# Kernel optimization log

Measured on AMD Instinct MI355X. Metric: run time of the kernel, lower is better.

Reference implementation:

```python
import jax, jax.numpy as jnp
import numpy as np

HIDDEN_STATE_CLAMP = 4.0
MAX_REVIEW_LENGTH = 200
B, T, D_IN, D_H, D_OUT = 1024, 200, 300, 256, 2


def setup_inputs() -> dict:
    key = jax.random.key(0)
    k_x, k_wh, k_bh, k_wo, k_bo = jax.random.split(key, 5)
    fan_h = D_IN + D_H
    inputs = jax.random.normal(k_x, (B, T, D_IN), dtype=jnp.float32)
    # torch nn.Linear init: U(-1/sqrt(fan_in), 1/sqrt(fan_in)); stored as [in, out] here
    Wh = jax.random.uniform(k_wh, (fan_h, D_H), jnp.float32, -1.0, 1.0) / np.sqrt(fan_h)
    bh = jax.random.uniform(k_bh, (D_H,), jnp.float32, -1.0, 1.0) / np.sqrt(fan_h)
    Wo = jax.random.uniform(k_wo, (D_H, D_OUT), jnp.float32, -1.0, 1.0) / np.sqrt(D_H)
    bo = jax.random.uniform(k_bo, (D_OUT,), jnp.float32, -1.0, 1.0) / np.sqrt(D_H)
    return {"inputs": inputs, "Wh": Wh, "bh": bh, "Wo": Wo, "bo": bo}


def reference(inputs, Wh, bh, Wo, bo):
    # inputs: [B, T, D_in]; process at most MAX_REVIEW_LENGTH timesteps
    x_t = jnp.swapaxes(inputs[:, :MAX_REVIEW_LENGTH], 0, 1)  # [T, B, D_in]
    h0 = jnp.zeros((inputs.shape[0], Wh.shape[1]), dtype=inputs.dtype)

    def step(h, xt):
        combined = jnp.concatenate([xt, h], axis=-1)          # [B, D_in+D_h]
        pre = combined @ Wh + bh
        h = jnp.tanh(jnp.clip(pre, -HIDDEN_STATE_CLAMP, HIDDEN_STATE_CLAMP))
        return h, None

    h_final, _ = jax.lax.scan(step, h0, x_t)
    pre_out = jnp.clip(h_final @ Wo + bo, -HIDDEN_STATE_CLAMP, HIDDEN_STATE_CLAMP)
    return jax.nn.log_softmax(pre_out, axis=-1)
```

## Files before the change

kernel.cpp:

```cpp
#include <hip/hip_runtime.h>
#include <stdint.h>


typedef short s16x8 __attribute__((ext_vector_type(8)));
typedef float f32x4 __attribute__((ext_vector_type(4)));

__device__ __forceinline__ unsigned short f2bf(float f){
  uint32_t u = __builtin_bit_cast(uint32_t, f);
  u += 0x7fffu + ((u >> 16) & 1u);
  return (unsigned short)(u >> 16);
}
__device__ __forceinline__ float bf2f(unsigned short s){
  uint32_t u = ((uint32_t)s) << 16;
  return __builtin_bit_cast(float, u);
}
__device__ __forceinline__ uint32_t pack2(float a, float b){
  return (uint32_t)f2bf(a) | ((uint32_t)f2bf(b) << 16);
}

__global__ void prep_kernel(const float* __restrict__ Wh,
                            unsigned short* __restrict__ wxf,
                            unsigned short* __restrict__ whhf){
  int id = blockIdx.x * 256 + threadIdx.x;
  if (id < 81920){
    int j = id & 7, lane = (id >> 3) & 63, rem = id >> 9;
    int ki = rem % 10, CT = rem / 10;
    int k = ki * 32 + ((lane >> 4) << 3) + j;
    int col = CT * 16 + (lane & 15);
    wxf[id] = (k < 300) ? f2bf(Wh[k * 256 + col]) : (unsigned short)0;
  } else if (id < 81920 + 65536){
    int id2 = id - 81920;
    int j = id2 & 7, lane = (id2 >> 3) & 63, rem = id2 >> 9;
    int ki = rem & 7, CT = rem >> 3;
    int k = ki * 32 + ((lane >> 4) << 3) + j;
    int col = CT * 16 + (lane & 15);
    whhf[id2] = f2bf(Wh[(300 + k) * 256 + col]);
  }
}

__global__ __launch_bounds__(512, 4) void phase1_kernel(
    const float* __restrict__ x, const float* __restrict__ bh,
    const unsigned short* __restrict__ wxf, unsigned short* __restrict__ U){
  __shared__ unsigned short hx[128 * 320];
  int blk = blockIdx.x;
  int bt = blk / 25;
  int t0 = (blk - bt * 25) * 8;
  int tid = threadIdx.x;
  int w = tid >> 6, l = tid & 63;
  int m = l & 15, kg = l >> 4;

  const float4* xb = (const float4*)x + (long)(bt * 16) * 15000 + t0 * 75;
  for (int i = tid; i < 9600; i += 512){
    int bl = i / 600;
    int j  = i - bl * 600;
    float4 v = xb[(long)bl * 15000 + j];
    int tt = j / 75;
    int k4 = j - tt * 75;
    int idx = (((tt * 16 + bl) * 320) + k4 * 4) ^ ((bl & 7) << 3);
    *(uint2*)(&hx[idx]) = make_uint2(pack2(v.x, v.y), pack2(v.z, v.w));
  }
  for (int i = tid; i < 640; i += 512){
    int r = i / 5, q = i - r * 5;
    int idx = (r * 320 + 300 + q * 4) ^ ((r & 7) << 3);
    *(uint2*)(&hx[idx]) = make_uint2(0u, 0u);
  }

  s16x8 Bf0[10], Bf1[10];
  const unsigned short* w0p = wxf + (2 * w + 0) * 5120 + l * 8;
  const unsigned short* w1p = wxf + (2 * w + 1) * 5120 + l * 8;
#pragma unroll
  for (int ki = 0; ki < 10; ki++){
    Bf0[ki] = *(const s16x8*)(w0p + ki * 512);
    Bf1[ki] = *(const s16x8*)(w1p + ki * 512);
  }
  float b0 = bh[w * 32 + m], b1 = bh[w * 32 + 16 + m];
  __syncthreads();

  unsigned short* ub = U + (long)bt * 819200 + (long)t0 * 4096 + (w * 64 + l) * 8;
  int abase = m * 320 + kg * 8;
  int swz = (m & 7) << 3;
#pragma unroll 1
  for (int tt = 0; tt < 8; tt++){
    f32x4 acc0 = {b0, b0, b0, b0};
    f32x4 acc1 = {b1, b1, b1, b1};
    int ab = tt * 5120 + abase;
#pragma unroll
    for (int ki = 0; ki < 10; ki++){
      s16x8 a = *(const s16x8*)(&hx[(ab + ki * 32) ^ swz]);
      acc0 = __builtin_amdgcn_mfma_f32_16x16x32_bf16(a, Bf0[ki], acc0, 0, 0, 0);
      acc1 = __builtin_amdgcn_mfma_f32_16x16x32_bf16(a, Bf1[ki], acc1, 0, 0, 0);
    }
    s16x8 o;
#pragma unroll
    for (int r = 0; r < 4; r++){
      o[r]     = (short)f2bf(acc0[r]);
      o[4 + r] = (short)f2bf(acc1[r]);
    }
    *(s16x8*)(ub + tt * 4096) = o;
  }
}

__global__ __launch_bounds__(512) void phase2_kernel(
    const unsigned short* __restrict__ U, const unsigned short* __restrict__ whhf,
    const float* __restrict__ Wo, const float* __restrict__ bo,
    float* __restrict__ out){
  __shared__ unsigned short h2[2][16 * 264];
  __shared__ float flds[16][257];
  int bt = blockIdx.x;
  int tid = threadIdx.x;
  int w = tid >> 6, l = tid & 63;
  int m = l & 15, kg = l >> 4;

  s16x8 Bf0[8], Bf1[8];
#pragma unroll
  for (int ki = 0; ki < 8; ki++){
    Bf0[ki] = *(const s16x8*)(whhf + ((2 * w + 0) * 8 + ki) * 512 + l * 8);
    Bf1[ki] = *(const s16x8*)(whhf + ((2 * w + 1) * 8 + ki) * 512 + l * 8);
  }
  for (int i = tid; i < 16 * 264; i += 512) h2[0][i] = 0;
  const unsigned short* ubase = U + (long)bt * 819200 + (w * 64 + l) * 8;
  s16x8 u = *(const s16x8*)ubase;
  __syncthreads();

  float hk[8];
  int p = 0;
  for (int t = 0; t < 200; t++){
    f32x4 acc0, acc1;
    f32x4 acc0b = {0.f, 0.f, 0.f, 0.f}, acc1b = {0.f, 0.f, 0.f, 0.f};
#pragma unroll
    for (int r = 0; r < 4; r++){
      acc0[r] = bf2f((unsigned short)u[r]);
      acc1[r] = bf2f((unsigned short)u[4 + r]);
    }
    int tn = (t < 199) ? t + 1 : 199;
    s16x8 un = *(const s16x8*)(ubase + (long)tn * 4096);
    s16x8 a[8];
#pragma unroll
    for (int ki = 0; ki < 8; ki++)
      a[ki] = *(const s16x8*)(&h2[p][m * 264 + ki * 32 + kg * 8]);
#pragma unroll
    for (int ki = 0; ki < 4; ki++){
      acc0  = __builtin_amdgcn_mfma_f32_16x16x32_bf16(a[ki],     Bf0[ki],     acc0,  0, 0, 0);
      acc1  = __builtin_amdgcn_mfma_f32_16x16x32_bf16(a[ki],     Bf1[ki],     acc1,  0, 0, 0);
      acc0b = __builtin_amdgcn_mfma_f32_16x16x32_bf16(a[ki + 4], Bf0[ki + 4], acc0b, 0, 0, 0);
      acc1b = __builtin_amdgcn_mfma_f32_16x16x32_bf16(a[ki + 4], Bf1[ki + 4], acc1b, 0, 0, 0);
    }
#pragma unroll
    for (int i = 0; i < 8; i++){
      float pre = (i < 4) ? (acc0[i] + acc0b[i]) : (acc1[i - 4] + acc1b[i - 4]);
      float c = fminf(fmaxf(pre, -4.f), 4.f);
      float e = __expf(2.f * c);
      float h = 1.f - 2.f * __builtin_amdgcn_rcpf(e + 1.f);
      hk[i] = h;
      int r = i & 3, ct = i >> 2;
      h2[p ^ 1][(kg * 4 + r) * 264 + w * 32 + ct * 16 + m] = f2bf(h);
    }
    __syncthreads();
    p ^= 1;
    u = un;
  }

#pragma unroll
  for (int i = 0; i < 8; i++){
    int r = i & 3, ct = i >> 2;
    flds[kg * 4 + r][w * 32 + ct * 16 + m] = hk[i];
  }
  __syncthreads();
  int rr = tid >> 5, q = tid & 31;
  float p0 = 0.f, p1 = 0.f;
#pragma unroll
  for (int j = 0; j < 8; j++){
    float hv = flds[rr][q + 32 * j];
    p0 += hv * Wo[(q + 32 * j) * 2 + 0];
    p1 += hv * Wo[(q + 32 * j) * 2 + 1];
  }
#pragma unroll
  for (int mm = 16; mm >= 1; mm >>= 1){
    p0 += __shfl_xor(p0, mm, 32);
    p1 += __shfl_xor(p1, mm, 32);
  }
  if (q == 0){
    p0 = fminf(fmaxf(p0 + bo[0], -4.f), 4.f);
    p1 = fminf(fmaxf(p1 + bo[1], -4.f), 4.f);
    float mx = fmaxf(p0, p1);
    float lse = mx + logf(__expf(p0 - mx) + __expf(p1 - mx));
    int orow = bt * 16 + rr;
    out[orow * 2 + 0] = p0 - lse;
    out[orow * 2 + 1] = p1 - lse;
  }
}

extern "C" void kernel_launch(void* const* d_in, const int* in_sizes, int n_in,
                              void* d_out, int out_size, void* d_ws, size_t ws_size,
                              hipStream_t stream){
  const float* x  = (const float*)d_in[0];
  const float* Wh = (const float*)d_in[1];
  const float* bh = (const float*)d_in[2];
  const float* Wo = (const float*)d_in[3];
  const float* bo = (const float*)d_in[4];
  float* out = (float*)d_out;

  unsigned short* U    = (unsigned short*)d_ws;
  unsigned short* wxf  = (unsigned short*)((char*)d_ws + 104857600);
  unsigned short* whhf = (unsigned short*)((char*)d_ws + 104857600 + 163840);

  prep_kernel<<<576, 256, 0, stream>>>(Wh, wxf, whhf);
  phase1_kernel<<<1600, 512, 0, stream>>>(x, bh, wxf, U);
  phase2_kernel<<<64, 512, 0, stream>>>(U, whhf, Wo, bo, out);
}
```

Measured before the change: 240.6 us.

## Transpose recurrent MFMA operands and use 4 waves per block in phase2

Swaps the A/B operands of the MFMAs so each lane holds 4 consecutive hidden columns of one batch row, and re-lays out U to match. Phase2 now uses 4 waves of 256 threads, each computing 4 column tiles (64 columns), so every MFMA reuses the same A fragment. It also writes h back to LDS as packed 8-byte stores and prefetches U two steps ahead. The aim is to cut per-step LDS traffic and barrier cost on the serial recurrence. In exchange, each wave issues twice as many dependent MFMAs per step and holds 32 weight fragments in registers.

```diff
diff --git a/kernel.cpp b/kernel.cpp
--- a/kernel.cpp
+++ b/kernel.cpp
@@ -73,118 +73,126 @@
     Bf0[ki] = *(const s16x8*)(w0p + ki * 512);
     Bf1[ki] = *(const s16x8*)(w1p + ki * 512);
   }
-  float b0 = bh[w * 32 + m], b1 = bh[w * 32 + 16 + m];
+  float4 bv0 = *(const float4*)(bh + (2 * w + 0) * 16 + kg * 4);
+  float4 bv1 = *(const float4*)(bh + (2 * w + 1) * 16 + kg * 4);
   __syncthreads();
 
-  unsigned short* ub = U + (long)bt * 819200 + (long)t0 * 4096 + (w * 64 + l) * 8;
   int abase = m * 320 + kg * 8;
   int swz = (m & 7) << 3;
 #pragma unroll 1
   for (int tt = 0; tt < 8; tt++){
-    f32x4 acc0 = {b0, b0, b0, b0};
-    f32x4 acc1 = {b1, b1, b1, b1};
+    f32x4 acc0 = {bv0.x, bv0.y, bv0.z, bv0.w};
+    f32x4 acc1 = {bv1.x, bv1.y, bv1.z, bv1.w};
     int ab = tt * 5120 + abase;
 #pragma unroll
     for (int ki = 0; ki < 10; ki++){
       s16x8 a = *(const s16x8*)(&hx[(ab + ki * 32) ^ swz]);
-      acc0 = __builtin_amdgcn_mfma_f32_16x16x32_bf16(a, Bf0[ki], acc0, 0, 0, 0);
-      acc1 = __builtin_amdgcn_mfma_f32_16x16x32_bf16(a, Bf1[ki], acc1, 0, 0, 0);
-    }
-    s16x8 o;
-#pragma unroll
-    for (int r = 0; r < 4; r++){
-      o[r]     = (short)f2bf(acc0[r]);
-      o[4 + r] = (short)f2bf(acc1[r]);
-    }
-    *(s16x8*)(ub + tt * 4096) = o;
-  }
-}
-
-__global__ __launch_bounds__(512) void phase2_kernel(
+      acc0 = __builtin_amdgcn_mfma_f32_16x16x32_bf16(Bf0[ki], a, acc0, 0, 0, 0);
+      acc1 = __builtin_amdgcn_mfma_f32_16x16x32_bf16(Bf1[ki], a, acc1, 0, 0, 0);
+    }
+    long base = (long)(bt * 200 + t0 + tt) * 4096;
+    uint2 s0 = make_uint2(pack2(acc0[0], acc0[1]), pack2(acc0[2], acc0[3]));
+    uint2 s1 = make_uint2(pack2(acc1[0], acc1[1]), pack2(acc1[2], acc1[3]));
+    int o0 = (w >> 1) * 1024 + l * 16 + ((w & 1) * 2 + 0) * 4;
+    int o1 = (w >> 1) * 1024 + l * 16 + ((w & 1) * 2 + 1) * 4;
+    *(uint2*)(U + base + o0) = s0;
+    *(uint2*)(U + base + o1) = s1;
+  }
+}
+
+__global__ __launch_bounds__(256, 1) void phase2_kernel(
     const unsigned short* __restrict__ U, const unsigned short* __restrict__ whhf,
     const float* __restrict__ Wo, const float* __restrict__ bo,
     float* __restrict__ out){
-  __shared__ unsigned short h2[2][16 * 264];
-  __shared__ float flds[16][257];
+  __shared__ unsigned short h2[2][16 * 272];
+  __shared__ float flds[16][272];
   int bt = blockIdx.x;
   int tid = threadIdx.x;
   int w = tid >> 6, l = tid & 63;
-  int m = l & 15, kg = l >> 4;
-
-  s16x8 Bf0[8], Bf1[8];
-#pragma unroll
-  for (int ki = 0; ki < 8; ki++){
-    Bf0[ki] = *(const s16x8*)(whhf + ((2 * w + 0) * 8 + ki) * 512 + l * 8);
-    Bf1[ki] = *(const s16x8*)(whhf + ((2 * w + 1) * 8 + ki) * 512 + l * 8);
-  }
-  for (int i = tid; i < 16 * 264; i += 512) h2[0][i] = 0;
-  const unsigned short* ubase = U + (long)bt * 819200 + (w * 64 + l) * 8;
-  s16x8 u = *(const s16x8*)ubase;
+  int n = l & 15, kg = l >> 4;
+
+  s16x8 Bf[4][8];
+#pragma unroll
+  for (int tt = 0; tt < 4; tt++)
+#pragma unroll
+    for (int ki = 0; ki < 8; ki++)
+      Bf[tt][ki] = *(const s16x8*)(whhf + ((4 * w + tt) * 8 + ki) * 512 + l * 8);
+
+  for (int i = tid; i < 16 * 272; i += 256) h2[0][i] = 0;
+
+  const unsigned short* ub = U + (long)bt * 819200 + w * 1024 + l * 16;
+  s16x8 u0c = *(const s16x8*)(ub);
+  s16x8 u1c = *(const s16x8*)(ub + 8);
+  s16x8 u0n = *(const s16x8*)(ub + 4096);
+  s16x8 u1n = *(const s16x8*)(ub + 4096 + 8);
   __syncthreads();
 
-  float hk[8];
+  float hv[16];
   int p = 0;
   for (int t = 0; t < 200; t++){
-    f32x4 acc0, acc1;
-    f32x4 acc0b = {0.f, 0.f, 0.f, 0.f}, acc1b = {0.f, 0.f, 0.f, 0.f};
+    int tf = (t < 198) ? t + 2 : 199;
+    s16x8 u0f = *(const s16x8*)(ub + (long)tf * 4096);
+    s16x8 u1f = *(const s16x8*)(ub + (long)tf * 4096 + 8);
+
+    s16x8 a[8];
+#pragma unroll
+    for (int ki = 0; ki < 8; ki++)
+      a[ki] = *(const s16x8*)(&h2[p][n * 272 + ki * 32 + kg * 8]);
+
+    f32x4 acc[4];
 #pragma unroll
     for (int r = 0; r < 4; r++){
-      acc0[r] = bf2f((unsigned short)u[r]);
-      acc1[r] = bf2f((unsigned short)u[4 + r]);
-    }
-    int tn = (t < 199) ? t + 1 : 199;
-    s16x8 un = *(const s16x8*)(ubase + (long)tn * 4096);
-    s16x8 a[8];
-#pragma unroll
-    for (int ki = 0; ki < 8; ki++)
-      a[ki] = *(const s16x8*)(&h2[p][m * 264 + ki * 32 + kg * 8]);
-#pragma unroll
-    for (int ki = 0; ki < 4; ki++){
-      acc0  = __builtin_amdgcn_mfma_f32_16x16x32_bf16(a[ki],     Bf0[ki],     acc0,  0, 0, 0);
-      acc1  = __builtin_amdgcn_mfma_f32_16x16x32_bf16(a[ki],     Bf1[ki],     acc1,  0, 0, 0);
-      acc0b = __builtin_amdgcn_mfma_f32_16x16x32_bf16(a[ki + 4], Bf0[ki + 4], acc0b, 0, 0, 0);
-      acc1b = __builtin_amdgcn_mfma_f32_16x16x32_bf16(a[ki + 4], Bf1[ki + 4], acc1b, 0, 0, 0);
-    }
-#pragma unroll
-    for (int i = 0; i < 8; i++){
-      float pre = (i < 4) ? (acc0[i] + acc0b[i]) : (acc1[i - 4] + acc1b[i - 4]);
-      float c = fminf(fmaxf(pre, -4.f), 4.f);
+      acc[0][r] = bf2f((unsigned short)u0c[r]);
+      acc[1][r] = bf2f((unsigned short)u0c[4 + r]);
+      acc[2][r] = bf2f((unsigned short)u1c[r]);
+      acc[3][r] = bf2f((unsigned short)u1c[4 + r]);
+    }
+#pragma unroll
+    for (int ki = 0; ki < 8; ki++){
+#pragma unroll
+      for (int tt = 0; tt < 4; tt++)
+        acc[tt] = __builtin_amdgcn_mfma_f32_16x16x32_bf16(Bf[tt][ki], a[ki], acc[tt], 0, 0, 0);
+    }
+#pragma unroll
+    for (int i = 0; i < 16; i++){
+      float c = fminf(fmaxf(acc[i >> 2][i & 3], -4.f), 4.f);
       float e = __expf(2.f * c);
-      float h = 1.f - 2.f * __builtin_amdgcn_rcpf(e + 1.f);
-      hk[i] = h;
-      int r = i & 3, ct = i >> 2;
-      h2[p ^ 1][(kg * 4 + r) * 264 + w * 32 + ct * 16 + m] = f2bf(h);
+      hv[i] = 1.f - 2.f * __builtin_amdgcn_rcpf(e + 1.f);
+    }
+#pragma unroll
+    for (int tt = 0; tt < 4; tt++){
+      uint2 d = make_uint2(pack2(hv[tt * 4], hv[tt * 4 + 1]),
+                           pack2(hv[tt * 4 + 2], hv[tt * 4 + 3]));
+      *(uint2*)(&h2[p ^ 1][n * 272 + (4 * w + tt) * 16 + kg * 4]) = d;
     }
     __syncthreads();
     p ^= 1;
-    u = un;
-  }
-
-#pragma unroll
-  for (int i = 0; i < 8; i++){
-    int r = i & 3, ct = i >> 2;
-    flds[kg * 4 + r][w * 32 + ct * 16 + m] = hk[i];
-  }
+    u0c = u0n; u1c = u1n; u0n = u0f; u1n = u1f;
+  }
+
+#pragma unroll
+  for (int i = 0; i < 16; i++)
+    flds[n][(4 * w + (i >> 2)) * 16 + kg * 4 + (i & 3)] = hv[i];
   __syncthreads();
-  int rr = tid >> 5, q = tid & 31;
+  int row = tid >> 4, q = tid & 15;
   float p0 = 0.f, p1 = 0.f;
 #pragma unroll
-  for (int j = 0; j < 8; j++){
-    float hv = flds[rr][q + 32 * j];
-    p0 += hv * Wo[(q + 32 * j) * 2 + 0];
-    p1 += hv * Wo[(q + 32 * j) * 2 + 1];
-  }
-#pragma unroll
-  for (int mm = 16; mm >= 1; mm >>= 1){
-    p0 += __shfl_xor(p0, mm, 32);
-    p1 += __shfl_xor(p1, mm, 32);
+  for (int jj = 0; jj < 16; jj++){
+    float hvv = flds[row][q + 16 * jj];
+    p0 += hvv * Wo[(q + 16 * jj) * 2 + 0];
+    p1 += hvv * Wo[(q + 16 * jj) * 2 + 1];
+  }
+#pragma unroll
+  for (int mm = 8; mm >= 1; mm >>= 1){
+    p0 += __shfl_xor(p0, mm, 16);
+    p1 += __shfl_xor(p1, mm, 16);
   }
   if (q == 0){
     p0 = fminf(fmaxf(p0 + bo[0], -4.f), 4.f);
     p1 = fminf(fmaxf(p1 + bo[1], -4.f), 4.f);
     float mx = fmaxf(p0, p1);
     float lse = mx + logf(__expf(p0 - mx) + __expf(p1 - mx));
-    int orow = bt * 16 + rr;
+    int orow = bt * 16 + row;
     out[orow * 2 + 0] = p0 - lse;
     out[orow * 2 + 1] = p1 - lse;
   }
@@ -206,5 +214,5 @@
 
   prep_kernel<<<576, 256, 0, stream>>>(Wh, wxf, whhf);
   phase1_kernel<<<1600, 512, 0, stream>>>(x, bh, wxf, U);
-  phase2_kernel<<<64, 512, 0, stream>>>(U, whhf, Wo, bo, out);
-}
+  phase2_kernel<<<64, 256, 0, stream>>>(U, whhf, Wo, bo, out);
+}
```

After: 297.3 us. 1.24x slower.

## Transpose MFMA operands so each lane holds 4 contiguous hidden columns and prefetch U two steps ahead

Applied to the files above, without the earlier changes.

Both kernels swap the MFMA A/B operands so the accumulator holds four consecutive output columns per lane for one batch row. This allows vectorized bias loads, packed 64-bit LDS stores of the new hidden state (replacing eight scalar 16-bit stores), and a matching U layout. Phase 2 also prefetches U two timesteps ahead, pins the weight fragments in registers, and changes the LDS row pitch to 272. The aim is to shorten the serial per-step critical path in the recurrence, which costs more registers and may change bank-conflict behaviour.

```diff
diff --git a/kernel.cpp b/kernel.cpp
--- a/kernel.cpp
+++ b/kernel.cpp
@@ -73,43 +73,43 @@
     Bf0[ki] = *(const s16x8*)(w0p + ki * 512);
     Bf1[ki] = *(const s16x8*)(w1p + ki * 512);
   }
-  float b0 = bh[w * 32 + m], b1 = bh[w * 32 + 16 + m];
+  float4 bv0 = *(const float4*)(bh + (2 * w + 0) * 16 + kg * 4);
+  float4 bv1 = *(const float4*)(bh + (2 * w + 1) * 16 + kg * 4);
   __syncthreads();
 
-  unsigned short* ub = U + (long)bt * 819200 + (long)t0 * 4096 + (w * 64 + l) * 8;
   int abase = m * 320 + kg * 8;
   int swz = (m & 7) << 3;
 #pragma unroll 1
   for (int tt = 0; tt < 8; tt++){
-    f32x4 acc0 = {b0, b0, b0, b0};
-    f32x4 acc1 = {b1, b1, b1, b1};
+    f32x4 acc0 = {bv0.x, bv0.y, bv0.z, bv0.w};
+    f32x4 acc1 = {bv1.x, bv1.y, bv1.z, bv1.w};
     int ab = tt * 5120 + abase;
 #pragma unroll
     for (int ki = 0; ki < 10; ki++){
       s16x8 a = *(const s16x8*)(&hx[(ab + ki * 32) ^ swz]);
-      acc0 = __builtin_amdgcn_mfma_f32_16x16x32_bf16(a, Bf0[ki], acc0, 0, 0, 0);
-      acc1 = __builtin_amdgcn_mfma_f32_16x16x32_bf16(a, Bf1[ki], acc1, 0, 0, 0);
-    }
-    s16x8 o;
-#pragma unroll
-    for (int r = 0; r < 4; r++){
-      o[r]     = (short)f2bf(acc0[r]);
-      o[4 + r] = (short)f2bf(acc1[r]);
-    }
-    *(s16x8*)(ub + tt * 4096) = o;
-  }
-}
-
-__global__ __launch_bounds__(512) void phase2_kernel(
+      acc0 = __builtin_amdgcn_mfma_f32_16x16x32_bf16(Bf0[ki], a, acc0, 0, 0, 0);
+      acc1 = __builtin_amdgcn_mfma_f32_16x16x32_bf16(Bf1[ki], a, acc1, 0, 0, 0);
+    }
+    long base = (long)(bt * 200 + t0 + tt) * 4096;
+    uint4 s;
+    s.x = pack2(acc0[0], acc0[1]);
+    s.y = pack2(acc0[2], acc0[3]);
+    s.z = pack2(acc1[0], acc1[1]);
+    s.w = pack2(acc1[2], acc1[3]);
+    *(uint4*)(U + base + w * 512 + l * 8) = s;
+  }
+}
+
+__global__ __launch_bounds__(512, 2) void phase2_kernel(
     const unsigned short* __restrict__ U, const unsigned short* __restrict__ whhf,
     const float* __restrict__ Wo, const float* __restrict__ bo,
     float* __restrict__ out){
-  __shared__ unsigned short h2[2][16 * 264];
-  __shared__ float flds[16][257];
+  __shared__ unsigned short h2[2][16 * 272];
+  __shared__ float flds[16][272];
   int bt = blockIdx.x;
   int tid = threadIdx.x;
   int w = tid >> 6, l = tid & 63;
-  int m = l & 15, kg = l >> 4;
+  int n = l & 15, kg = l >> 4;
 
   s16x8 Bf0[8], Bf1[8];
 #pragma unroll
@@ -117,62 +117,75 @@
     Bf0[ki] = *(const s16x8*)(whhf + ((2 * w + 0) * 8 + ki) * 512 + l * 8);
     Bf1[ki] = *(const s16x8*)(whhf + ((2 * w + 1) * 8 + ki) * 512 + l * 8);
   }
-  for (int i = tid; i < 16 * 264; i += 512) h2[0][i] = 0;
-  const unsigned short* ubase = U + (long)bt * 819200 + (w * 64 + l) * 8;
-  s16x8 u = *(const s16x8*)ubase;
+#pragma unroll
+  for (int ki = 0; ki < 8; ki++){
+    asm volatile("" : "+v"(Bf0[ki]));
+    asm volatile("" : "+v"(Bf1[ki]));
+  }
+
+  for (int i = tid; i < 16 * 272; i += 512) h2[0][i] = 0;
+
+  const unsigned short* ub = U + (long)bt * 819200 + w * 512 + l * 8;
+  s16x8 uc = *(const s16x8*)(ub);
+  s16x8 un = *(const s16x8*)(ub + 4096);
   __syncthreads();
 
-  float hk[8];
+  float hv[8];
   int p = 0;
   for (int t = 0; t < 200; t++){
-    f32x4 acc0, acc1;
+    int tf = (t < 198) ? t + 2 : 199;
+    s16x8 uf = *(const s16x8*)(ub + (long)tf * 4096);
+
+    s16x8 a[8];
+#pragma unroll
+    for (int ki = 0; ki < 8; ki++)
+      a[ki] = *(const s16x8*)(&h2[p][n * 272 + ki * 32 + kg * 8]);
+
+    f32x4 acc0a, acc1a;
     f32x4 acc0b = {0.f, 0.f, 0.f, 0.f}, acc1b = {0.f, 0.f, 0.f, 0.f};
 #pragma unroll
     for (int r = 0; r < 4; r++){
-      acc0[r] = bf2f((unsigned short)u[r]);
-      acc1[r] = bf2f((unsigned short)u[4 + r]);
-    }
-    int tn = (t < 199) ? t + 1 : 199;
-    s16x8 un = *(const s16x8*)(ubase + (long)tn * 4096);
-    s16x8 a[8];
-#pragma unroll
-    for (int ki = 0; ki < 8; ki++)
-      a[ki] = *(const s16x8*)(&h2[p][m * 264 + ki * 32 + kg * 8]);
+      acc0a[r] = bf2f((unsigned short)uc[r]);
+      acc1a[r] = bf2f((unsigned short)uc[4 + r]);
+    }
 #pragma unroll
     for (int ki = 0; ki < 4; ki++){
-      acc0  = __builtin_amdgcn_mfma_f32_16x16x32_bf16(a[ki],     Bf0[ki],     acc0,  0, 0, 0);
-      acc1  = __builtin_amdgcn_mfma_f32_16x16x32_bf16(a[ki],     Bf1[ki],     acc1,  0, 0, 0);
-      acc0b = __builtin_amdgcn_mfma_f32_16x16x32_bf16(a[ki + 4], Bf0[ki + 4], acc0b, 0, 0, 0);
-      acc1b = __builtin_amdgcn_mfma_f32_16x16x32_bf16(a[ki + 4], Bf1[ki + 4], acc1b, 0, 0, 0);
+      acc0a = __builtin_amdgcn_mfma_f32_16x16x32_bf16(Bf0[ki],     a[ki],     acc0a, 0, 0, 0);
+      acc1a = __builtin_amdgcn_mfma_f32_16x16x32_bf16(Bf1[ki],     a[ki],     acc1a, 0, 0, 0);
+      acc0b = __builtin_amdgcn_mfma_f32_16x16x32_bf16(Bf0[ki + 4], a[ki + 4], acc0b, 0, 0, 0);
+      acc1b = __builtin_amdgcn_mfma_f32_16x16x32_bf16(Bf1[ki + 4], a[ki + 4], acc1b, 0, 0, 0);
     }
 #pragma unroll
     for (int i = 0; i < 8; i++){
-      float pre = (i < 4) ? (acc0[i] + acc0b[i]) : (acc1[i - 4] + acc1b[i - 4]);
+      float pre = (i < 4) ? (acc0a[i] + acc0b[i]) : (acc1a[i - 4] + acc1b[i - 4]);
       float c = fminf(fmaxf(pre, -4.f), 4.f);
       float e = __expf(2.f * c);
-      float h = 1.f - 2.f * __builtin_amdgcn_rcpf(e + 1.f);
-      hk[i] = h;
-      int r = i & 3, ct = i >> 2;
-      h2[p ^ 1][(kg * 4 + r) * 264 + w * 32 + ct * 16 + m] = f2bf(h);
+      hv[i] = 1.f - 2.f * __builtin_amdgcn_rcpf(e + 1.f);
+    }
+    {
+      uint2 d0 = make_uint2(pack2(hv[0], hv[1]), pack2(hv[2], hv[3]));
+      uint2 d1 = make_uint2(pack2(hv[4], hv[5]), pack2(hv[6], hv[7]));
+      *(uint2*)(&h2[p ^ 1][n * 272 + (2 * w + 0) * 16 + kg * 4]) = d0;
+      *(uint2*)(&h2[p ^ 1][n * 272 + (2 * w + 1) * 16 + kg * 4]) = d1;
     }
     __syncthreads();
     p ^= 1;
-    u = un;
+    uc = un; un = uf;
   }
 
 #pragma unroll
   for (int i = 0; i < 8; i++){
-    int r = i & 3, ct = i >> 2;
-    flds[kg * 4 + r][w * 32 + ct * 16 + m] = hk[i];
+    int r = i & 3, c = i >> 2;
+    flds[n][(2 * w + c) * 16 + kg * 4 + r] = hv[i];
   }
   __syncthreads();
-  int rr = tid >> 5, q = tid & 31;
+  int row = tid >> 5, q = tid & 31;
   float p0 = 0.f, p1 = 0.f;
 #pragma unroll
-  for (int j = 0; j < 8; j++){
-    float hv = flds[rr][q + 32 * j];
-    p0 += hv * Wo[(q + 32 * j) * 2 + 0];
-    p1 += hv * Wo[(q + 32 * j) * 2 + 1];
+  for (int jj = 0; jj < 8; jj++){
+    float hvv = flds[row][q + 32 * jj];
+    p0 += hvv * Wo[(q + 32 * jj) * 2 + 0];
+    p1 += hvv * Wo[(q + 32 * jj) * 2 + 1];
   }
 #pragma unroll
   for (int mm = 16; mm >= 1; mm >>= 1){
@@ -184,7 +197,7 @@
     p1 = fminf(fmaxf(p1 + bo[1], -4.f), 4.f);
     float mx = fmaxf(p0, p1);
     float lse = mx + logf(__expf(p0 - mx) + __expf(p1 - mx));
-    int orow = bt * 16 + rr;
+    int orow = bt * 16 + row;
     out[orow * 2 + 0] = p0 - lse;
     out[orow * 2 + 1] = p1 - lse;
   }
```

Result: no change. 244.0 us (+1.4%).
